# Kernel optimization log

Measured on AMD Instinct MI355X. Metric: run time of the kernel, lower is better.

The kernel has to match this reference:

```python
import jax, jax.numpy as jnp
import numpy as np

B, T, V, L = 131072, 6, 31, 3  # batch, seq_len, vocab/hidden, num RNN layers


def setup_inputs() -> dict:
    key = jax.random.key(0)
    ks = jax.random.split(key, 8)
    s = 1.0 / np.sqrt(V)  # torch default init scale for RNN/Linear
    return {
        "inp": jax.random.normal(ks[0], (B, T, V), dtype=jnp.float32),
        "h0": jax.random.normal(ks[1], (L, B, V), dtype=jnp.float32),
        "W_ih": jax.random.uniform(ks[2], (L, V, V), jnp.float32, -s, s),
        "W_hh": jax.random.uniform(ks[3], (L, V, V), jnp.float32, -s, s),
        "b_ih": jax.random.uniform(ks[4], (L, V), jnp.float32, -s, s),
        "b_hh": jax.random.uniform(ks[5], (L, V), jnp.float32, -s, s),
        "W_lin": jax.random.uniform(ks[6], (V, V), jnp.float32, -s, s),
        "b_lin": jax.random.uniform(ks[7], (V,), jnp.float32, -s, s),
    }


def _rnn_layer(x_tm, h0_l, wih, whh, bih, bhh):
    # x_tm: [T, B, V] time-major; h0_l: [B, V]
    def step(h, x_t):
        h_new = jnp.tanh(x_t @ wih.T + bih + h @ whh.T + bhh)
        return h_new, h_new

    _, ys = jax.lax.scan(step, h0_l, x_tm)
    return ys  # [T, B, V]


def reference(inp, h0, W_ih, W_hh, b_ih, b_hh, W_lin, b_lin):
    x = jnp.transpose(inp, (1, 0, 2))  # [T, B, V] time-major
    for l in range(L):
        x = _rnn_layer(x, h0[l], W_ih[l], W_hh[l], b_ih[l], b_hh[l])
    y = jnp.tanh(x @ W_lin.T + b_lin)  # [T, B, V]
    last = y[-1]  # [B, V] == y[:, -1, :] in batch-major
    return jax.nn.softmax(last, axis=1)
```

## Files before the change

### kernel.cpp

```cpp
#include <hip/hip_runtime.h>
#include <hip/hip_bf16.h>


#define VD 31
#define TD 6

typedef __attribute__((ext_vector_type(8))) short bf16x8;
typedef __attribute__((ext_vector_type(4))) float f32x4;
typedef __attribute__((ext_vector_type(4))) unsigned u32x4;
typedef float f32x4u __attribute__((ext_vector_type(4), aligned(4)));

struct raw8 { f32x4u a, b; };

__device__ __forceinline__ short f2bf(float f) {
    unsigned u = __float_as_uint(f);
    unsigned r = (u + 0x7fffu + ((u >> 16) & 1u)) >> 16;
    return (short)r;
}

__device__ __forceinline__ unsigned f2bf2u(float lo, float hi) {
    union { __hip_bfloat162 h2; unsigned u; } cvt;
    cvt.h2 = __float22bfloat162_rn(make_float2(lo, hi));
    return cvt.u;
}

__device__ __forceinline__ float fast_tanh(float x) {
    x = fminf(fmaxf(x, -15.0f), 15.0f);
    float e = __expf(2.0f * x);
    return (e - 1.0f) * __builtin_amdgcn_rcpf(e + 1.0f);
}

__device__ __forceinline__ raw8 load_raw(const float* __restrict__ p, int fo) {
    raw8 r;
    r.a = *(const f32x4u*)(p + fo);
    r.b = *(const f32x4u*)(p + fo + 4);
    return r;
}

__device__ __forceinline__ bf16x8 cvt_frag(raw8 r, bool q3) {
    float l[8] = {r.a[0], r.a[1], r.a[2], r.a[3], r.b[0], r.b[1], r.b[2], r.b[3]};
    float s[8];
#pragma unroll
    for (int j = 0; j < 7; ++j) s[j] = q3 ? l[j + 1] : l[j];
    s[7] = q3 ? 1.0f : l[7];
    union { u32x4 u4; bf16x8 b8; } cvt;
#pragma unroll
    for (int j = 0; j < 4; ++j) cvt.u4[j] = f2bf2u(s[2 * j], s[2 * j + 1]);
    return cvt.b8;
}

__device__ __forceinline__ bf16x8 load_wfrag(const float* __restrict__ W,
                                             const float* __restrict__ b1,
                                             const float* __restrict__ b2,
                                             int i, int half, int k0) {
    const int nn = 8 * (i >> 2) + (i & 3) + 4 * half;
    bf16x8 r;
#pragma unroll
    for (int j = 0; j < 8; ++j) {
        int k = k0 + j;
        float v = 0.0f;
        if (nn < VD) {
            if (k < VD) v = W[nn * VD + k];
            else v = (b1 ? b1[nn] : 0.0f) + (b2 ? b2[nn] : 0.0f);
        }
        r[j] = f2bf(v);
    }
    return r;
}

__device__ __forceinline__ bf16x8 layer_step(bf16x8 x, bf16x8 h,
    bf16x8 wi0, bf16x8 wi1, bf16x8 wh0, bf16x8 wh1, bool q3)
{
    const f32x4 z = {0.0f, 0.0f, 0.0f, 0.0f};
    f32x4 c0 = __builtin_amdgcn_mfma_f32_16x16x32_bf16(wh0, h, z, 0, 0, 0);
    f32x4 c1 = __builtin_amdgcn_mfma_f32_16x16x32_bf16(wh1, h, z, 0, 0, 0);
    c0 = __builtin_amdgcn_mfma_f32_16x16x32_bf16(wi0, x, c0, 0, 0, 0);
    c1 = __builtin_amdgcn_mfma_f32_16x16x32_bf16(wi1, x, c1, 0, 0, 0);
    float t0 = fast_tanh(c0[0]), t1 = fast_tanh(c0[1]);
    float t2 = fast_tanh(c0[2]), t3 = fast_tanh(c0[3]);
    float t4 = fast_tanh(c1[0]), t5 = fast_tanh(c1[1]);
    float t6 = fast_tanh(c1[2]);
    float t7 = q3 ? 1.0f : fast_tanh(c1[3]);
    union { u32x4 u4; bf16x8 b8; } cvt;
    cvt.u4[0] = f2bf2u(t0, t1);
    cvt.u4[1] = f2bf2u(t2, t3);
    cvt.u4[2] = f2bf2u(t4, t5);
    cvt.u4[3] = f2bf2u(t6, t7);
    return cvt.b8;
}

__global__ __launch_bounds__(256, 1) void rnn_mfma(
    const float* __restrict__ inp,
    const float* __restrict__ h0,
    const float* __restrict__ Wih,
    const float* __restrict__ Whh,
    const float* __restrict__ bih,
    const float* __restrict__ bhh,
    const float* __restrict__ Wlin,
    const float* __restrict__ blin,
    float* __restrict__ out,
    int B)
{
    const int wave = threadIdx.x >> 6;
    const int lane = threadIdx.x & 63;
    const int cb   = lane & 15;
    const int quad = lane >> 4;
    const int k0   = quad * 8;
    const bool q3  = (quad == 3);
    const int fo   = q3 ? 23 : k0;
    const int bbase = (blockIdx.x * 4 + wave) * 32;
    if (bbase >= B) return;

    const float* W0 = Wih;               const float* U0 = Whh;
    const float* W1 = Wih + VD * VD;     const float* U1 = Whh + VD * VD;
    const float* W2 = Wih + 2 * VD * VD; const float* U2 = Whh + 2 * VD * VD;
    const bf16x8 wiA0 = load_wfrag(W0, bih, bhh, cb, 0, k0);
    const bf16x8 wiA1 = load_wfrag(W0, bih, bhh, cb, 1, k0);
    const bf16x8 whA0 = load_wfrag(U0, nullptr, nullptr, cb, 0, k0);
    const bf16x8 whA1 = load_wfrag(U0, nullptr, nullptr, cb, 1, k0);
    const bf16x8 wiB0 = load_wfrag(W1, bih + VD, bhh + VD, cb, 0, k0);
    const bf16x8 wiB1 = load_wfrag(W1, bih + VD, bhh + VD, cb, 1, k0);
    const bf16x8 whB0 = load_wfrag(U1, nullptr, nullptr, cb, 0, k0);
    const bf16x8 whB1 = load_wfrag(U1, nullptr, nullptr, cb, 1, k0);
    const bf16x8 wiC0 = load_wfrag(W2, bih + 2 * VD, bhh + 2 * VD, cb, 0, k0);
    const bf16x8 wiC1 = load_wfrag(W2, bih + 2 * VD, bhh + 2 * VD, cb, 1, k0);
    const bf16x8 whC0 = load_wfrag(U2, nullptr, nullptr, cb, 0, k0);
    const bf16x8 whC1 = load_wfrag(U2, nullptr, nullptr, cb, 1, k0);
    const bf16x8 wl0  = load_wfrag(Wlin, blin, nullptr, cb, 0, k0);
    const bf16x8 wl1  = load_wfrag(Wlin, blin, nullptr, cb, 1, k0);

    bf16x8 h1a = cvt_frag(load_raw(h0 + ((size_t)0 * B + bbase + cb) * VD, fo), q3);
    bf16x8 h1b = cvt_frag(load_raw(h0 + ((size_t)0 * B + bbase + 16 + cb) * VD, fo), q3);
    bf16x8 h2a = cvt_frag(load_raw(h0 + ((size_t)1 * B + bbase + cb) * VD, fo), q3);
    bf16x8 h2b = cvt_frag(load_raw(h0 + ((size_t)1 * B + bbase + 16 + cb) * VD, fo), q3);
    bf16x8 h3a = cvt_frag(load_raw(h0 + ((size_t)2 * B + bbase + cb) * VD, fo), q3);
    bf16x8 h3b = cvt_frag(load_raw(h0 + ((size_t)2 * B + bbase + 16 + cb) * VD, fo), q3);

    const float* xrow0 = inp + (size_t)(bbase + cb) * TD * VD;
    const float* xrow1 = inp + (size_t)(bbase + 16 + cb) * TD * VD;

    raw8 rx0 = load_raw(xrow0, fo);
    raw8 rx1 = load_raw(xrow1, fo);

    for (int t = 0; t < TD; ++t) {
        bf16x8 ax0 = cvt_frag(rx0, q3);
        bf16x8 ax1 = cvt_frag(rx1, q3);
        if (t + 1 < TD) {
            rx0 = load_raw(xrow0 + (t + 1) * VD, fo);
            rx1 = load_raw(xrow1 + (t + 1) * VD, fo);
        }
        h1a = layer_step(ax0, h1a, wiA0, wiA1, whA0, whA1, q3);
        h1b = layer_step(ax1, h1b, wiA0, wiA1, whA0, whA1, q3);
        h2a = layer_step(h1a, h2a, wiB0, wiB1, whB0, whB1, q3);
        h2b = layer_step(h1b, h2b, wiB0, wiB1, whB0, whB1, q3);
        h3a = layer_step(h2a, h3a, wiC0, wiC1, whC0, whC1, q3);
        h3b = layer_step(h2b, h3b, wiC0, wiC1, whC0, whC1, q3);
    }

    const f32x4 z = {0.0f, 0.0f, 0.0f, 0.0f};
#pragma unroll
    for (int tb = 0; tb < 2; ++tb) {
        bf16x8 h3 = tb ? h3b : h3a;
        f32x4 c0 = __builtin_amdgcn_mfma_f32_16x16x32_bf16(wl0, h3, z, 0, 0, 0);
        f32x4 c1 = __builtin_amdgcn_mfma_f32_16x16x32_bf16(wl1, h3, z, 0, 0, 0);
        float v0 = fast_tanh(c0[0]), v1 = fast_tanh(c0[1]);
        float v2 = fast_tanh(c0[2]), v3 = fast_tanh(c0[3]);
        float v4 = fast_tanh(c1[0]), v5 = fast_tanh(c1[1]);
        float v6 = fast_tanh(c1[2]), v7 = fast_tanh(c1[3]);
        float mx = fmaxf(fmaxf(fmaxf(v0, v1), fmaxf(v2, v3)),
                         fmaxf(fmaxf(v4, v5), fmaxf(v6, v7)));
        mx = fmaxf(mx, __shfl_xor(mx, 16));
        mx = fmaxf(mx, __shfl_xor(mx, 32));
        float e0 = __expf(v0 - mx), e1 = __expf(v1 - mx);
        float e2 = __expf(v2 - mx), e3 = __expf(v3 - mx);
        float e4 = __expf(v4 - mx), e5 = __expf(v5 - mx);
        float e6 = __expf(v6 - mx);
        float e7 = q3 ? 0.0f : __expf(v7 - mx);
        float s = ((e0 + e1) + (e2 + e3)) + ((e4 + e5) + (e6 + e7));
        s += __shfl_xor(s, 16);
        s += __shfl_xor(s, 32);
        const float inv = __builtin_amdgcn_rcpf(s);
        const size_t row = (size_t)(bbase + tb * 16 + cb);
        float* po = out + row * VD + k0;
        f32x4u lo = {e0 * inv, e1 * inv, e2 * inv, e3 * inv};
        *(f32x4u*)po = lo;
        if (!q3) {
            f32x4u hi = {e4 * inv, e5 * inv, e6 * inv, e7 * inv};
            *(f32x4u*)(po + 4) = hi;
        } else {
            po[4] = e4 * inv;
            po[5] = e5 * inv;
            po[6] = e6 * inv;
        }
    }
}

extern "C" void kernel_launch(void* const* d_in, const int* in_sizes, int n_in,
                              void* d_out, int out_size, void* d_ws, size_t ws_size,
                              hipStream_t stream) {
    const float* inp  = (const float*)d_in[0];
    const float* h0   = (const float*)d_in[1];
    const float* Wih  = (const float*)d_in[2];
    const float* Whh  = (const float*)d_in[3];
    const float* bih  = (const float*)d_in[4];
    const float* bhh  = (const float*)d_in[5];
    const float* Wlin = (const float*)d_in[6];
    const float* blin = (const float*)d_in[7];
    float* out = (float*)d_out;

    const int B = in_sizes[0] / (TD * VD);
    const int grid = (B + 127) / 128;
    rnn_mfma<<<grid, 256, 0, stream>>>(inp, h0, Wih, Whh, bih, bhh, Wlin, blin, out, B);
}
```

Before: 215.1 us.

## Fold tanh scale into weights and wavefront-pipeline the three RNN layers

Weights and biases are prescaled by 2/ln2 so tanh becomes a single exp2, reciprocal and fma, with no clamp and no multiply per element. The time loop is also reordered into a wavefront over layers and fully unrolled, so layer 3 at step t-2, layer 2 at step t-1 and layer 1 at step t are independent and their MFMA and transcendental latencies can overlap. The new tanh relies on exp2 overflowing to inf, which gives 1/(inf+1)=0, to saturate correctly. Full unrolling grows code size and register pressure.

Result: slower. 227.3 us (+5.7%).

```diff
diff --git a/kernel.cpp b/kernel.cpp
--- a/kernel.cpp
+++ b/kernel.cpp
@@ -4,6 +4,7 @@
 
 #define VD 31
 #define TD 6
+#define SCL 2.8853900817779268f
 
 typedef __attribute__((ext_vector_type(8))) short bf16x8;
 typedef __attribute__((ext_vector_type(4))) float f32x4;
@@ -24,10 +25,18 @@
     return cvt.u;
 }
 
-__device__ __forceinline__ float fast_tanh(float x) {
-    x = fminf(fmaxf(x, -15.0f), 15.0f);
-    float e = __expf(2.0f * x);
-    return (e - 1.0f) * __builtin_amdgcn_rcpf(e + 1.0f);
+__device__ __forceinline__ float fexp2(float x) {
+#if __has_builtin(__builtin_amdgcn_exp2f)
+    return __builtin_amdgcn_exp2f(x);
+#else
+    float r; asm("v_exp_f32 %0, %1" : "=v"(r) : "v"(x)); return r;
+#endif
+}
+
+__device__ __forceinline__ float tanh_pre(float c) {
+    float e = fexp2(c);
+    float r = __builtin_amdgcn_rcpf(e + 1.0f);
+    return __builtin_fmaf(-2.0f, r, 1.0f);
 }
 
 __device__ __forceinline__ raw8 load_raw(const float* __restrict__ p, int fo) {
@@ -63,7 +72,7 @@
             if (k < VD) v = W[nn * VD + k];
             else v = (b1 ? b1[nn] : 0.0f) + (b2 ? b2[nn] : 0.0f);
         }
-        r[j] = f2bf(v);
+        r[j] = f2bf(v * SCL);
     }
     return r;
 }
@@ -76,11 +85,11 @@
     f32x4 c1 = __builtin_amdgcn_mfma_f32_16x16x32_bf16(wh1, h, z, 0, 0, 0);
     c0 = __builtin_amdgcn_mfma_f32_16x16x32_bf16(wi0, x, c0, 0, 0, 0);
     c1 = __builtin_amdgcn_mfma_f32_16x16x32_bf16(wi1, x, c1, 0, 0, 0);
-    float t0 = fast_tanh(c0[0]), t1 = fast_tanh(c0[1]);
-    float t2 = fast_tanh(c0[2]), t3 = fast_tanh(c0[3]);
-    float t4 = fast_tanh(c1[0]), t5 = fast_tanh(c1[1]);
-    float t6 = fast_tanh(c1[2]);
-    float t7 = q3 ? 1.0f : fast_tanh(c1[3]);
+    float t0 = tanh_pre(c0[0]), t1 = tanh_pre(c0[1]);
+    float t2 = tanh_pre(c0[2]), t3 = tanh_pre(c0[3]);
+    float t4 = tanh_pre(c1[0]), t5 = tanh_pre(c1[1]);
+    float t6 = tanh_pre(c1[2]);
+    float t7 = q3 ? 1.0f : tanh_pre(c1[3]);
     union { u32x4 u4; bf16x8 b8; } cvt;
     cvt.u4[0] = f2bf2u(t0, t1);
     cvt.u4[1] = f2bf2u(t2, t3);
@@ -142,19 +151,26 @@
     raw8 rx0 = load_raw(xrow0, fo);
     raw8 rx1 = load_raw(xrow1, fo);
 
-    for (int t = 0; t < TD; ++t) {
-        bf16x8 ax0 = cvt_frag(rx0, q3);
-        bf16x8 ax1 = cvt_frag(rx1, q3);
-        if (t + 1 < TD) {
-            rx0 = load_raw(xrow0 + (t + 1) * VD, fo);
-            rx1 = load_raw(xrow1 + (t + 1) * VD, fo);
-        }
-        h1a = layer_step(ax0, h1a, wiA0, wiA1, whA0, whA1, q3);
-        h1b = layer_step(ax1, h1b, wiA0, wiA1, whA0, whA1, q3);
-        h2a = layer_step(h1a, h2a, wiB0, wiB1, whB0, whB1, q3);
-        h2b = layer_step(h1b, h2b, wiB0, wiB1, whB0, whB1, q3);
-        h3a = layer_step(h2a, h3a, wiC0, wiC1, whC0, whC1, q3);
-        h3b = layer_step(h2b, h3b, wiC0, wiC1, whC0, whC1, q3);
+#pragma unroll
+    for (int v = 0; v < TD + 2; ++v) {
+        if (v >= 2) {
+            h3a = layer_step(h2a, h3a, wiC0, wiC1, whC0, whC1, q3);
+            h3b = layer_step(h2b, h3b, wiC0, wiC1, whC0, whC1, q3);
+        }
+        if (v >= 1 && v < TD + 1) {
+            h2a = layer_step(h1a, h2a, wiB0, wiB1, whB0, whB1, q3);
+            h2b = layer_step(h1b, h2b, wiB0, wiB1, whB0, whB1, q3);
+        }
+        if (v < TD) {
+            bf16x8 ax0 = cvt_frag(rx0, q3);
+            bf16x8 ax1 = cvt_frag(rx1, q3);
+            if (v + 1 < TD) {
+                rx0 = load_raw(xrow0 + (v + 1) * VD, fo);
+                rx1 = load_raw(xrow1 + (v + 1) * VD, fo);
+            }
+            h1a = layer_step(ax0, h1a, wiA0, wiA1, whA0, whA1, q3);
+            h1b = layer_step(ax1, h1b, wiA0, wiA1, whA0, whA1, q3);
+        }
     }
 
     const f32x4 z = {0.0f, 0.0f, 0.0f, 0.0f};
@@ -163,10 +179,10 @@
         bf16x8 h3 = tb ? h3b : h3a;
         f32x4 c0 = __builtin_amdgcn_mfma_f32_16x16x32_bf16(wl0, h3, z, 0, 0, 0);
         f32x4 c1 = __builtin_amdgcn_mfma_f32_16x16x32_bf16(wl1, h3, z, 0, 0, 0);
-        float v0 = fast_tanh(c0[0]), v1 = fast_tanh(c0[1]);
-        float v2 = fast_tanh(c0[2]), v3 = fast_tanh(c0[3]);
-        float v4 = fast_tanh(c1[0]), v5 = fast_tanh(c1[1]);
-        float v6 = fast_tanh(c1[2]), v7 = fast_tanh(c1[3]);
+        float v0 = tanh_pre(c0[0]), v1 = tanh_pre(c0[1]);
+        float v2 = tanh_pre(c0[2]), v3 = tanh_pre(c0[3]);
+        float v4 = tanh_pre(c1[0]), v5 = tanh_pre(c1[1]);
+        float v6 = tanh_pre(c1[2]), v7 = tanh_pre(c1[3]);
         float mx = fmaxf(fmaxf(fmaxf(v0, v1), fmaxf(v2, v3)),
                          fmaxf(fmaxf(v4, v5), fmaxf(v6, v7)));
         mx = fmaxf(mx, __shfl_xor(mx, 16));
```
